# Performance work log

Hardware: AMD Instinct MI355X
Metric: run time of the kernel (lower is better)

## Reference

```python
import jax, jax.numpy as jnp
import numpy as np


def setup_inputs() -> dict:
    key = jax.random.key(0)
    k1, k2 = jax.random.split(key)
    B, A, H, W, C = 4, 9, 256, 256, 9
    F = 64
    lfi = jax.random.normal(k1, (B, A, H, W, C), dtype=jnp.float32)
    f_maps = jax.random.uniform(k2, (B, H, W, F), dtype=jnp.float32)
    return {"lfi": lfi, "f_maps": f_maps}


def reference(lfi, f_maps):
    # height mask: per (b, filter), mean of the [h,w] map over rows, normalized by its max.
    # f_maps: [B, H, W, F] -> hv: [B, W, F]; note original asserts W == H.
    hv = jnp.mean(f_maps, axis=1)                      # [B, W, F]
    hv = hv / jnp.max(hv, axis=1, keepdims=True)       # normalize per (b, f)
    h_mask = jnp.transpose(hv, (0, 2, 1))              # [B, F, H]
    # lfi: [B, A, H, W, C]; h_feat[b,f] = lfi[b] * h_mask[b,f,:] broadcast over H axis,
    # then mean over angular dims A and C -> factorizes as mean(lfi) * h_mask.
    m = jnp.mean(lfi, axis=(1, 4))                     # [B, H, W]
    out = jnp.einsum('bhw,bfh->bhwf', m, h_mask)       # [B, H, W, F]
    return out
```

## Files before the change

### kernel.cpp

```cpp
#include <hip/hip_runtime.h>

#define BB 4
#define AA 9
#define HH 256
#define WW 256
#define CC 9
#define FF 64

__global__ __launch_bounds__(256) void k_hv(const float* __restrict__ fm,
                                            float* __restrict__ hv) {
    const int t = threadIdx.x;
    const int wq = blockIdx.x & 63;
    const int b = blockIdx.x >> 6;
    const int f4 = t & 15;
    const int wsub = (t >> 4) & 3;
    const int hl = t >> 6;
    const int w = wq * 4 + wsub;

    const float4* base = (const float4*)fm +
                         ((size_t)(b * HH + hl) * WW + w) * (FF / 4) + f4;
    const size_t hstep = (size_t)4 * WW * (FF / 4);
    float4 acc = make_float4(0.f, 0.f, 0.f, 0.f);
#pragma unroll 16
    for (int i = 0; i < 64; ++i) {
        float4 v = base[i * hstep];
        acc.x += v.x; acc.y += v.y; acc.z += v.z; acc.w += v.w;
    }

    __shared__ float4 sm[4][64];
    sm[hl][wsub * 16 + f4] = acc;
    __syncthreads();
    if (t < 64) {
        const float4 s0 = sm[0][t], s1 = sm[1][t], s2 = sm[2][t], s3 = sm[3][t];
        float4 r;
        r.x = ((s0.x + s1.x) + (s2.x + s3.x)) * (1.0f / HH);
        r.y = ((s0.y + s1.y) + (s2.y + s3.y)) * (1.0f / HH);
        r.z = ((s0.z + s1.z) + (s2.z + s3.z)) * (1.0f / HH);
        r.w = ((s0.w + s1.w) + (s2.w + s3.w)) * (1.0f / HH);
        ((float4*)hv)[(size_t)(b * WW + wq * 4 + (t >> 4)) * (FF / 4) + (t & 15)] = r;
    }
}

__global__ __launch_bounds__(256) void k_m(const float* __restrict__ lfi,
                                           const float* __restrict__ hv,
                                           float* __restrict__ m,
                                           float* __restrict__ inv) {
    const int t = threadIdx.x;
    if (blockIdx.x < 1024) {
        const int k = blockIdx.x * 256 + t;
        const int b = k >> 16;
        const int blk_local = blockIdx.x & 255;
        const int r = t & 3;
        const size_t astride4 = (size_t)HH * WW * CC / 4;

        const float4* base = (const float4*)lfi + (size_t)b * AA * astride4 +
                             (size_t)blk_local * 576 + ((9 * t) >> 2);
        float acc = 0.f;
#pragma unroll 3
        for (int a = 0; a < AA; ++a) {
            const float4* p = base + (size_t)a * astride4;
            const float4 v0 = p[0], v1 = p[1], v2 = p[2];
            const float s12 = ((v0.x + v0.y) + (v0.z + v0.w)) +
                              ((v1.x + v1.y) + (v1.z + v1.w)) +
                              ((v2.x + v2.y) + (v2.z + v2.w));
            const float head = (r > 0 ? v0.x : 0.f) + (r > 1 ? v0.y : 0.f) +
                               (r > 2 ? v0.z : 0.f);
            const float tail = (r < 1 ? v2.y : 0.f) + (r < 2 ? v2.z : 0.f) +
                               (r < 3 ? v2.w : 0.f);
            acc += s12 - head - tail;
        }
        m[k] = acc * (1.0f / (AA * CC));
    } else {
        const int rb = blockIdx.x - 1024;
        const int wave = t >> 6;
        const int lane = t & 63;
        const int pair = rb * 4 + wave;
        const int b = pair >> 6;
        const int f = pair & 63;
        float mx = -1e30f;
#pragma unroll
        for (int j = 0; j < 4; ++j) {
            mx = fmaxf(mx, hv[((size_t)b * WW + (lane + 64 * j)) * FF + f]);
        }
#pragma unroll
        for (int off = 32; off; off >>= 1)
            mx = fmaxf(mx, __shfl_xor(mx, off));
        if (lane == 0) inv[pair] = 1.0f / mx;
    }
}

__global__ __launch_bounds__(256) void k_out(const float* __restrict__ m,
                                             const float* __restrict__ hv,
                                             const float* __restrict__ inv,
                                             float4* __restrict__ out) {
    const int idx = blockIdx.x * 256 + threadIdx.x;
    const int f4 = idx & 15;
    const int rest = idx >> 4;
    const int h = (rest >> 8) & 255;
    const int b = rest >> 16;

    const float mv = m[rest];
    const float4 hv4 = ((const float4*)hv)[((size_t)(b * HH + h)) * (FF / 4) + f4];
    const float4 iv4 = ((const float4*)inv)[b * (FF / 4) + f4];

    float4 o;
    o.x = mv * hv4.x * iv4.x;
    o.y = mv * hv4.y * iv4.y;
    o.z = mv * hv4.z * iv4.z;
    o.w = mv * hv4.w * iv4.w;
    out[idx] = o;
}

extern "C" void kernel_launch(void* const* d_in, const int* in_sizes, int n_in,
                              void* d_out, int out_size, void* d_ws, size_t ws_size,
                              hipStream_t stream) {
    const float* lfi = (const float*)d_in[0];
    const float* fm  = (const float*)d_in[1];
    float* out = (float*)d_out;

    char* ws = (char*)d_ws;
    float* hv  = (float*)ws;
    float* inv = (float*)(ws + (size_t)BB * WW * FF * 4);
    float* m   = (float*)(ws + (size_t)BB * WW * FF * 4 + 1024);

    k_hv<<<BB * 64, 256, 0, stream>>>(fm, hv);
    k_m<<<1024 + 64, 256, 0, stream>>>(lfi, hv, m, inv);
    k_out<<<(BB * HH * WW * FF / 4) / 256, 256, 0, stream>>>(m, hv, inv,
                                                             (float4*)out);
}
```

Baseline: 42.44 us.

## Fuse column-mean and lfi-mean kernels, compute per-filter max via atomicMax

Merges the hv reduction and the lfi angular mean into one launch, so both run concurrently without a kernel boundary between them. The per-(b,f) max is computed inside the hv blocks with integer atomicMax on float bits, replacing the separate max-reduction blocks. The output kernel applies a hardware reciprocal on the fly. The integer-ordered max assumes non-negative hv values, and it adds a memset launch.

```diff
diff --git a/kernel.cpp b/kernel.cpp
--- a/kernel.cpp
+++ b/kernel.cpp
@@ -7,49 +7,66 @@
 #define CC 9
 #define FF 64
 
-__global__ __launch_bounds__(256) void k_hv(const float* __restrict__ fm,
-                                            float* __restrict__ hv) {
+__global__ __launch_bounds__(256) void k_fused(const float* __restrict__ fm,
+                                               const float* __restrict__ lfi,
+                                               float* __restrict__ hv,
+                                               int* __restrict__ mxb,
+                                               float* __restrict__ m) {
     const int t = threadIdx.x;
-    const int wq = blockIdx.x & 63;
-    const int b = blockIdx.x >> 6;
-    const int f4 = t & 15;
-    const int wsub = (t >> 4) & 3;
-    const int hl = t >> 6;
-    const int w = wq * 4 + wsub;
+    if (blockIdx.x < 256) {
+        const int wq = blockIdx.x & 63;
+        const int b = blockIdx.x >> 6;
+        const int f4 = t & 15;
+        const int wsub = (t >> 4) & 3;
+        const int hl = t >> 6;
+        const int w = wq * 4 + wsub;
 
-    const float4* base = (const float4*)fm +
-                         ((size_t)(b * HH + hl) * WW + w) * (FF / 4) + f4;
-    const size_t hstep = (size_t)4 * WW * (FF / 4);
-    float4 acc = make_float4(0.f, 0.f, 0.f, 0.f);
+        const float4* base = (const float4*)fm +
+                             ((size_t)(b * HH + hl) * WW + w) * (FF / 4) + f4;
+        const size_t hstep = (size_t)4 * WW * (FF / 4);
+        float4 acc = make_float4(0.f, 0.f, 0.f, 0.f);
 #pragma unroll 16
-    for (int i = 0; i < 64; ++i) {
-        float4 v = base[i * hstep];
-        acc.x += v.x; acc.y += v.y; acc.z += v.z; acc.w += v.w;
-    }
+        for (int i = 0; i < 64; ++i) {
+            float4 v = base[i * hstep];
+            acc.x += v.x; acc.y += v.y; acc.z += v.z; acc.w += v.w;
+        }
 
-    __shared__ float4 sm[4][64];
-    sm[hl][wsub * 16 + f4] = acc;
-    __syncthreads();
-    if (t < 64) {
-        const float4 s0 = sm[0][t], s1 = sm[1][t], s2 = sm[2][t], s3 = sm[3][t];
-        float4 r;
-        r.x = ((s0.x + s1.x) + (s2.x + s3.x)) * (1.0f / HH);
-        r.y = ((s0.y + s1.y) + (s2.y + s3.y)) * (1.0f / HH);
-        r.z = ((s0.z + s1.z) + (s2.z + s3.z)) * (1.0f / HH);
-        r.w = ((s0.w + s1.w) + (s2.w + s3.w)) * (1.0f / HH);
-        ((float4*)hv)[(size_t)(b * WW + wq * 4 + (t >> 4)) * (FF / 4) + (t & 15)] = r;
-    }
-}
-
-__global__ __launch_bounds__(256) void k_m(const float* __restrict__ lfi,
-                                           const float* __restrict__ hv,
-                                           float* __restrict__ m,
-                                           float* __restrict__ inv) {
-    const int t = threadIdx.x;
-    if (blockIdx.x < 1024) {
-        const int k = blockIdx.x * 256 + t;
+        __shared__ float4 sm[4][64];
+        __shared__ float4 smw[4][16];
+        sm[hl][wsub * 16 + f4] = acc;
+        __syncthreads();
+        if (t < 64) {
+            const float4 s0 = sm[0][t], s1 = sm[1][t];
+            const float4 s2 = sm[2][t], s3 = sm[3][t];
+            float4 r;
+            r.x = ((s0.x + s1.x) + (s2.x + s3.x)) * (1.0f / HH);
+            r.y = ((s0.y + s1.y) + (s2.y + s3.y)) * (1.0f / HH);
+            r.z = ((s0.z + s1.z) + (s2.z + s3.z)) * (1.0f / HH);
+            r.w = ((s0.w + s1.w) + (s2.w + s3.w)) * (1.0f / HH);
+            ((float4*)hv)[(size_t)(b * WW + wq * 4 + (t >> 4)) * (FF / 4) +
+                          (t & 15)] = r;
+            smw[t >> 4][t & 15] = r;
+        }
+        __syncthreads();
+        if (t < 16) {
+            const float4 a0 = smw[0][t], a1 = smw[1][t];
+            const float4 a2 = smw[2][t], a3 = smw[3][t];
+            float4 mx;
+            mx.x = fmaxf(fmaxf(a0.x, a1.x), fmaxf(a2.x, a3.x));
+            mx.y = fmaxf(fmaxf(a0.y, a1.y), fmaxf(a2.y, a3.y));
+            mx.z = fmaxf(fmaxf(a0.z, a1.z), fmaxf(a2.z, a3.z));
+            mx.w = fmaxf(fmaxf(a0.w, a1.w), fmaxf(a2.w, a3.w));
+            int* mp = mxb + b * FF + t * 4;
+            atomicMax(mp + 0, __float_as_int(mx.x));
+            atomicMax(mp + 1, __float_as_int(mx.y));
+            atomicMax(mp + 2, __float_as_int(mx.z));
+            atomicMax(mp + 3, __float_as_int(mx.w));
+        }
+    } else {
+        const int blkm = blockIdx.x - 256;
+        const int k = blkm * 256 + t;
         const int b = k >> 16;
-        const int blk_local = blockIdx.x & 255;
+        const int blk_local = blkm & 255;
         const int r = t & 3;
         const size_t astride4 = (size_t)HH * WW * CC / 4;
 
@@ -70,28 +87,12 @@
             acc += s12 - head - tail;
         }
         m[k] = acc * (1.0f / (AA * CC));
-    } else {
-        const int rb = blockIdx.x - 1024;
-        const int wave = t >> 6;
-        const int lane = t & 63;
-        const int pair = rb * 4 + wave;
-        const int b = pair >> 6;
-        const int f = pair & 63;
-        float mx = -1e30f;
-#pragma unroll
-        for (int j = 0; j < 4; ++j) {
-            mx = fmaxf(mx, hv[((size_t)b * WW + (lane + 64 * j)) * FF + f]);
-        }
-#pragma unroll
-        for (int off = 32; off; off >>= 1)
-            mx = fmaxf(mx, __shfl_xor(mx, off));
-        if (lane == 0) inv[pair] = 1.0f / mx;
     }
 }
 
 __global__ __launch_bounds__(256) void k_out(const float* __restrict__ m,
                                              const float* __restrict__ hv,
-                                             const float* __restrict__ inv,
+                                             const int* __restrict__ mxb,
                                              float4* __restrict__ out) {
     const int idx = blockIdx.x * 256 + threadIdx.x;
     const int f4 = idx & 15;
@@ -101,13 +102,13 @@
 
     const float mv = m[rest];
     const float4 hv4 = ((const float4*)hv)[((size_t)(b * HH + h)) * (FF / 4) + f4];
-    const float4 iv4 = ((const float4*)inv)[b * (FF / 4) + f4];
+    const int4 mx4 = ((const int4*)mxb)[b * (FF / 4) + f4];
 
     float4 o;
-    o.x = mv * hv4.x * iv4.x;
-    o.y = mv * hv4.y * iv4.y;
-    o.z = mv * hv4.z * iv4.z;
-    o.w = mv * hv4.w * iv4.w;
+    o.x = mv * hv4.x * __builtin_amdgcn_rcpf(__int_as_float(mx4.x));
+    o.y = mv * hv4.y * __builtin_amdgcn_rcpf(__int_as_float(mx4.y));
+    o.z = mv * hv4.z * __builtin_amdgcn_rcpf(__int_as_float(mx4.z));
+    o.w = mv * hv4.w * __builtin_amdgcn_rcpf(__int_as_float(mx4.w));
     out[idx] = o;
 }
 
@@ -119,12 +120,12 @@
     float* out = (float*)d_out;
 
     char* ws = (char*)d_ws;
-    float* hv  = (float*)ws;
-    float* inv = (float*)(ws + (size_t)BB * WW * FF * 4);
-    float* m   = (float*)(ws + (size_t)BB * WW * FF * 4 + 1024);
+    float* hv = (float*)ws;
+    int* mxb  = (int*)(ws + (size_t)BB * WW * FF * 4);
+    float* m  = (float*)(ws + (size_t)BB * WW * FF * 4 + 4096);
 
-    k_hv<<<BB * 64, 256, 0, stream>>>(fm, hv);
-    k_m<<<1024 + 64, 256, 0, stream>>>(lfi, hv, m, inv);
-    k_out<<<(BB * HH * WW * FF / 4) / 256, 256, 0, stream>>>(m, hv, inv,
+    hipMemsetAsync(mxb, 0, BB * FF * sizeof(int), stream);
+    k_fused<<<256 + 1024, 256, 0, stream>>>(fm, lfi, hv, mxb, m);
+    k_out<<<(BB * HH * WW * FF / 4) / 256, 256, 0, stream>>>(m, hv, mxb,
                                                              (float4*)out);
 }
```

Result: slower. 47.27 us (+11.4%).
